# Kernel optimization log

Measured on AMD Instinct MI355X. Metric: run time of the kernel, lower is better.

The kernel has to match this reference:

```python
import jax, jax.numpy as jnp
import numpy as np

K, N_PER, D_IN, D_OUT = 16, 16384, 256, 256
N = K * N_PER


def setup_inputs() -> dict:
    key = jax.random.key(0)
    k1, k2, k3 = jax.random.split(key, 3)
    x = jax.random.normal(k1, (K, N_PER, D_IN), dtype=jnp.float32)
    w = jax.random.normal(k2, (K, D_OUT, D_IN), dtype=jnp.float32) * (1.0 / np.sqrt(D_IN))
    # collect order: permutation mapping grouped-by-type rows -> global neuron order
    perm = jax.random.permutation(k3, N).astype(jnp.int32)
    return {"x": x, "w": w, "perm": perm}


def reference(x, w, perm):
    # per-type unique linear: y[k,n,o] = sum_d x[k,n,d] * w[k,o,d]
    y = jnp.einsum('knd,kod->kno', x, w)          # [K, N_PER, D_OUT]
    y = y.reshape(N, D_OUT)[perm]                 # collect into unified neuron order
    return jnp.tanh(y)
```

## Files before the change

kernel.cpp:

```cpp
#include <hip/hip_runtime.h>
#include <hip/hip_bf16.h>

#define KT    16
#define NPER  16384
#define DIN   256
#define DOUT  256
#define NTOT  (KT * NPER)

typedef __attribute__((ext_vector_type(8))) short  short8;
typedef __attribute__((ext_vector_type(4))) float  f32x4;
typedef __attribute__((ext_vector_type(4))) unsigned int uint32x4;

__device__ __forceinline__ unsigned short f2bf(float f) {
    unsigned int u = __float_as_uint(f);
    u += 0x7fffu + ((u >> 16) & 1u);
    return (unsigned short)(u >> 16);
}

__device__ __forceinline__ float fast_tanh(float y) {
    float a = fabsf(y);
    float t = __expf(-2.0f * a);
    float r = (1.0f - t) * __builtin_amdgcn_rcpf(1.0f + t);
    return copysignf(r, y);
}


__global__ void prep_w(const float* __restrict__ w, unsigned short* __restrict__ wbf) {
    int i = blockIdx.x * blockDim.x + threadIdx.x;
    float4 v = ((const float4*)w)[i];
    unsigned int p0 = (unsigned int)f2bf(v.x) | ((unsigned int)f2bf(v.y) << 16);
    unsigned int p1 = (unsigned int)f2bf(v.z) | ((unsigned int)f2bf(v.w) << 16);
    ((uint2*)wbf)[i] = make_uint2(p0, p1);
}

__global__ void prep_inv(const int* __restrict__ perm, int* __restrict__ inv) {
    int i = blockIdx.x * blockDim.x + threadIdx.x;
    inv[perm[i]] = i;
}


__launch_bounds__(512, 4)
__global__ void gemm_scatter(const float* __restrict__ x,
                             const unsigned short* __restrict__ wbf,
                             const int* __restrict__ inv,
                             float* __restrict__ out) {
    __shared__ unsigned short aLds[128 * 72];
    __shared__ unsigned short bLds[256 * 72];
    __shared__ int invLds[128];

    const int tid = threadIdx.x;
    const int bid = blockIdx.x;
    const int kt  = bid >> 7;
    const int rt  = bid & 127;

    const float*          xblk = x   + (size_t)(kt * NPER + rt * 128) * DIN;
    const unsigned short* wblk = wbf + (size_t)kt * DOUT * DIN;

    if (tid < 128) invLds[tid] = inv[kt * NPER + rt * 128 + tid];

    const int lane = tid & 63;
    const int wv   = tid >> 6;
    const int wm   = wv & 1;
    const int wn   = wv >> 1;
    const int lo   = lane & 15;
    const int hi   = lane >> 4;

    f32x4 acc[4][4];
#pragma unroll
    for (int i = 0; i < 4; i++)
#pragma unroll
        for (int j = 0; j < 4; j++) acc[i][j] = (f32x4){0.f, 0.f, 0.f, 0.f};

    for (int s = 0; s < 4; ++s) {
        const int d0 = s * 64;

#pragma unroll
        for (int r8 = 0; r8 < 2; r8++) {
            int idx = tid + r8 * 512;
            int row = idx >> 3, c8 = idx & 7;
            const float4* p = (const float4*)(xblk + row * DIN + d0 + c8 * 8);
            float4 v0 = p[0];
            float4 v1 = p[1];
            uint32x4 pk;
            pk.x = (unsigned int)f2bf(v0.x) | ((unsigned int)f2bf(v0.y) << 16);
            pk.y = (unsigned int)f2bf(v0.z) | ((unsigned int)f2bf(v0.w) << 16);
            pk.z = (unsigned int)f2bf(v1.x) | ((unsigned int)f2bf(v1.y) << 16);
            pk.w = (unsigned int)f2bf(v1.z) | ((unsigned int)f2bf(v1.w) << 16);
            *(uint32x4*)&aLds[row * 72 + c8 * 8] = pk;
        }
#pragma unroll
        for (int r8 = 0; r8 < 4; r8++) {
            int idx = tid + r8 * 512;
            int row = idx >> 3, c8 = idx & 7;
            uint32x4 v = *(const uint32x4*)(wblk + row * DIN + d0 + c8 * 8);
            *(uint32x4*)&bLds[row * 72 + c8 * 8] = v;
        }
        __syncthreads();

#pragma unroll
        for (int ks = 0; ks < 2; ++ks) {
            const int k0 = ks * 32;
            short8 af[4], bfr[4];
#pragma unroll
            for (int i = 0; i < 4; i++)
                af[i] = *(const short8*)&aLds[(wm * 64 + i * 16 + lo) * 72 + k0 + hi * 8];
#pragma unroll
            for (int j = 0; j < 4; j++)
                bfr[j] = *(const short8*)&bLds[(wn * 64 + j * 16 + lo) * 72 + k0 + hi * 8];
#pragma unroll
            for (int i = 0; i < 4; i++)
#pragma unroll
                for (int j = 0; j < 4; j++)
                    acc[i][j] = __builtin_amdgcn_mfma_f32_16x16x32_bf16(
                        af[i], bfr[j], acc[i][j], 0, 0, 0);
        }
        __syncthreads();
    }

#pragma unroll
    for (int i = 0; i < 4; i++) {
#pragma unroll
        for (int r = 0; r < 4; r++) {
            int rowL = wm * 64 + i * 16 + hi * 4 + r;
            size_t orow = (size_t)invLds[rowL];
            float* op = out + orow * DOUT;
#pragma unroll
            for (int j = 0; j < 4; j++) {
                int col = wn * 64 + j * 16 + lo;
                op[col] = fast_tanh(acc[i][j][r]);
            }
        }
    }
}


extern "C" void kernel_launch(void* const* d_in, const int* in_sizes, int n_in,
                              void* d_out, int out_size, void* d_ws, size_t ws_size,
                              hipStream_t stream) {
    const float* x    = (const float*)d_in[0];
    const float* w    = (const float*)d_in[1];
    const int*   perm = (const int*)d_in[2];
    float*       out  = (float*)d_out;

    unsigned short* wbf = (unsigned short*)d_ws;
    int*            inv = (int*)((char*)d_ws + (size_t)2 * 1024 * 1024);

    prep_w  <<<1024, 256, 0, stream>>>(w, wbf);
    prep_inv<<<1024, 256, 0, stream>>>(perm, inv);
    gemm_scatter<<<KT * 128, 512, 0, stream>>>(x, wbf, inv, out);
}
```

Before: 457.5 us.

## Double-buffer LDS with register prefetch over K=32 steps, nontemporal output stores

Splits the K loop into eight 32-wide steps using double-buffered LDS tiles. Global loads for the next step go into registers before the MFMAs and are written to the alternate buffer afterwards, so only one barrier is needed per step. The aim is to hide global-load latency behind compute. The scattered tanh output now uses nontemporal stores to reduce cache pollution. The cost is more registers for the prefetch and more barrier iterations.

```diff
diff --git a/kernel.cpp b/kernel.cpp
--- a/kernel.cpp
+++ b/kernel.cpp
@@ -11,10 +11,10 @@
 typedef __attribute__((ext_vector_type(4))) float  f32x4;
 typedef __attribute__((ext_vector_type(4))) unsigned int uint32x4;
 
-__device__ __forceinline__ unsigned short f2bf(float f) {
+__device__ __forceinline__ unsigned int f2bf(float f) {
     unsigned int u = __float_as_uint(f);
     u += 0x7fffu + ((u >> 16) & 1u);
-    return (unsigned short)(u >> 16);
+    return u >> 16;
 }
 
 __device__ __forceinline__ float fast_tanh(float y) {
@@ -28,8 +28,8 @@
 __global__ void prep_w(const float* __restrict__ w, unsigned short* __restrict__ wbf) {
     int i = blockIdx.x * blockDim.x + threadIdx.x;
     float4 v = ((const float4*)w)[i];
-    unsigned int p0 = (unsigned int)f2bf(v.x) | ((unsigned int)f2bf(v.y) << 16);
-    unsigned int p1 = (unsigned int)f2bf(v.z) | ((unsigned int)f2bf(v.w) << 16);
+    unsigned int p0 = f2bf(v.x) | (f2bf(v.y) << 16);
+    unsigned int p1 = f2bf(v.z) | (f2bf(v.w) << 16);
     ((uint2*)wbf)[i] = make_uint2(p0, p1);
 }
 
@@ -39,13 +39,15 @@
 }
 
 
+#define PADK 40
+
 __launch_bounds__(512, 4)
 __global__ void gemm_scatter(const float* __restrict__ x,
                              const unsigned short* __restrict__ wbf,
                              const int* __restrict__ inv,
                              float* __restrict__ out) {
-    __shared__ unsigned short aLds[128 * 72];
-    __shared__ unsigned short bLds[256 * 72];
+    __shared__ unsigned short aLds[2 * 128 * PADK];
+    __shared__ unsigned short bLds[2 * 256 * PADK];
     __shared__ int invLds[128];
 
     const int tid = threadIdx.x;
@@ -71,50 +73,83 @@
 #pragma unroll
         for (int j = 0; j < 4; j++) acc[i][j] = (f32x4){0.f, 0.f, 0.f, 0.f};
 
-    for (int s = 0; s < 4; ++s) {
-        const int d0 = s * 64;
+    float4   pa[2];
+    uint32x4 pb[2];
 
 #pragma unroll
-        for (int r8 = 0; r8 < 2; r8++) {
-            int idx = tid + r8 * 512;
-            int row = idx >> 3, c8 = idx & 7;
-            const float4* p = (const float4*)(xblk + row * DIN + d0 + c8 * 8);
-            float4 v0 = p[0];
-            float4 v1 = p[1];
-            uint32x4 pk;
-            pk.x = (unsigned int)f2bf(v0.x) | ((unsigned int)f2bf(v0.y) << 16);
-            pk.y = (unsigned int)f2bf(v0.z) | ((unsigned int)f2bf(v0.w) << 16);
-            pk.z = (unsigned int)f2bf(v1.x) | ((unsigned int)f2bf(v1.y) << 16);
-            pk.w = (unsigned int)f2bf(v1.z) | ((unsigned int)f2bf(v1.w) << 16);
-            *(uint32x4*)&aLds[row * 72 + c8 * 8] = pk;
-        }
+    for (int it = 0; it < 2; it++) {
+        int idx = tid + it * 512, row = idx >> 3, c4 = idx & 7;
+        pa[it] = *(const float4*)(xblk + row * DIN + c4 * 4);
+    }
 #pragma unroll
-        for (int r8 = 0; r8 < 4; r8++) {
-            int idx = tid + r8 * 512;
-            int row = idx >> 3, c8 = idx & 7;
-            uint32x4 v = *(const uint32x4*)(wblk + row * DIN + d0 + c8 * 8);
-            *(uint32x4*)&bLds[row * 72 + c8 * 8] = v;
-        }
+    for (int it = 0; it < 2; it++) {
+        int idx = tid + it * 512, row = idx >> 2, c8 = idx & 3;
+        pb[it] = *(const uint32x4*)(wblk + row * DIN + c8 * 8);
+    }
+#pragma unroll
+    for (int it = 0; it < 2; it++) {
+        int idx = tid + it * 512, row = idx >> 3, c4 = idx & 7;
+        uint2 pk;
+        pk.x = f2bf(pa[it].x) | (f2bf(pa[it].y) << 16);
+        pk.y = f2bf(pa[it].z) | (f2bf(pa[it].w) << 16);
+        *(uint2*)&aLds[row * PADK + c4 * 4] = pk;
+    }
+#pragma unroll
+    for (int it = 0; it < 2; it++) {
+        int idx = tid + it * 512, row = idx >> 2, c8 = idx & 3;
+        *(uint32x4*)&bLds[row * PADK + c8 * 8] = pb[it];
+    }
+
+    for (int s = 0; s < 8; ++s) {
         __syncthreads();
 
+        if (s < 7) {
+            const int d1 = (s + 1) * 32;
 #pragma unroll
-        for (int ks = 0; ks < 2; ++ks) {
-            const int k0 = ks * 32;
-            short8 af[4], bfr[4];
+            for (int it = 0; it < 2; it++) {
+                int idx = tid + it * 512, row = idx >> 3, c4 = idx & 7;
+                pa[it] = *(const float4*)(xblk + row * DIN + d1 + c4 * 4);
+            }
 #pragma unroll
-            for (int i = 0; i < 4; i++)
-                af[i] = *(const short8*)&aLds[(wm * 64 + i * 16 + lo) * 72 + k0 + hi * 8];
+            for (int it = 0; it < 2; it++) {
+                int idx = tid + it * 512, row = idx >> 2, c8 = idx & 3;
+                pb[it] = *(const uint32x4*)(wblk + row * DIN + d1 + c8 * 8);
+            }
+        }
+
+        const unsigned short* aB = &aLds[(s & 1) * 128 * PADK];
+        const unsigned short* bB = &bLds[(s & 1) * 256 * PADK];
+        short8 af[4], bfr[4];
+#pragma unroll
+        for (int i = 0; i < 4; i++)
+            af[i] = *(const short8*)&aB[(wm * 64 + i * 16 + lo) * PADK + hi * 8];
+#pragma unroll
+        for (int j = 0; j < 4; j++)
+            bfr[j] = *(const short8*)&bB[(wn * 64 + j * 16 + lo) * PADK + hi * 8];
+#pragma unroll
+        for (int i = 0; i < 4; i++)
 #pragma unroll
             for (int j = 0; j < 4; j++)
-                bfr[j] = *(const short8*)&bLds[(wn * 64 + j * 16 + lo) * 72 + k0 + hi * 8];
+                acc[i][j] = __builtin_amdgcn_mfma_f32_16x16x32_bf16(
+                    af[i], bfr[j], acc[i][j], 0, 0, 0);
+
+        if (s < 7) {
+            unsigned short* aW = &aLds[((s + 1) & 1) * 128 * PADK];
+            unsigned short* bW = &bLds[((s + 1) & 1) * 256 * PADK];
 #pragma unroll
-            for (int i = 0; i < 4; i++)
+            for (int it = 0; it < 2; it++) {
+                int idx = tid + it * 512, row = idx >> 3, c4 = idx & 7;
+                uint2 pk;
+                pk.x = f2bf(pa[it].x) | (f2bf(pa[it].y) << 16);
+                pk.y = f2bf(pa[it].z) | (f2bf(pa[it].w) << 16);
+                *(uint2*)&aW[row * PADK + c4 * 4] = pk;
+            }
 #pragma unroll
-                for (int j = 0; j < 4; j++)
-                    acc[i][j] = __builtin_amdgcn_mfma_f32_16x16x32_bf16(
-                        af[i], bfr[j], acc[i][j], 0, 0, 0);
+            for (int it = 0; it < 2; it++) {
+                int idx = tid + it * 512, row = idx >> 2, c8 = idx & 3;
+                *(uint32x4*)&bW[row * PADK + c8 * 8] = pb[it];
+            }
         }
-        __syncthreads();
     }
 
 #pragma unroll
@@ -127,7 +162,7 @@
 #pragma unroll
             for (int j = 0; j < 4; j++) {
                 int col = wn * 64 + j * 16 + lo;
-                op[col] = fast_tanh(acc[i][j][r]);
+                __builtin_nontemporal_store(fast_tanh(acc[i][j][r]), op + col);
             }
         }
     }
```

After: 482.8 us. +5.5%, slower.
